# Performance work log

Measured on AMD Instinct MI355X. Metric: run time of the kernel, lower is better.

Reference implementation:

```python
import jax, jax.numpy as jnp
import numpy as np

N, E, IN, OUT, R, B = 20000, 640000, 256, 800, 8, 8


def setup_inputs() -> dict:
    key = jax.random.key(0)
    k0, k1, k2, k3, k4, k5 = jax.random.split(key, 6)
    x = jax.random.normal(k0, (N, IN), dtype=jnp.float32)
    edge_index = jax.random.randint(k1, (2, E), 0, N, dtype=jnp.int32)
    edge_type = jax.random.randint(k2, (E,), 0, R, dtype=jnp.int32)
    # basis-decomposed relation weights: W_r = sum_b att[r,b] * bases[b]
    bases = jax.random.normal(k3, (B, IN, OUT), dtype=jnp.float32) * 0.05
    att = jax.random.normal(k4, (R, B), dtype=jnp.float32) * 0.3
    root = jax.random.normal(k5, (IN, OUT), dtype=jnp.float32) * 0.05
    bias = jnp.zeros((OUT,), dtype=jnp.float32)
    return {"x": x, "edge_index": edge_index, "edge_type": edge_type,
            "bases": bases, "att": att, "root": root, "bias": bias}


def reference(x, edge_index, edge_type, bases, att, root, bias):
    # RGCNConv (basis decomposition, scatter-add aggregation):
    #   out[v] = sum_{(u->v, r) in edges} x[u] @ W_r  +  x[v] @ root  +  bias
    # Efficient form: first segment-sum x[src] per (dst, relation), then one
    # dense contraction with the R relation weights (math-identical for add-aggr).
    n, in_dim = x.shape
    r, b = att.shape
    W = jnp.einsum('rb,bio->rio', att, bases)          # [R, IN, OUT]
    src, dst = edge_index[0], edge_index[1]
    seg = dst.astype(jnp.int32) * r + edge_type.astype(jnp.int32)
    # per-(node, relation) sums of source features: [N*R, IN] -> [N, R, IN]
    s = jax.ops.segment_sum(x[src], seg, num_segments=n * r).reshape(n, r, in_dim)
    out = jnp.einsum('nri,rio->no', s, W) + x @ root + bias
    return out
```

## Files before the change

### kernel.cpp

```cpp
#include <hip/hip_runtime.h>


#define N_NODES 20000
#define N_EDGES 640000
#define IN_DIM  256
#define OUT_DIM 800
#define NREL    8
#define NSEG    160000
#define KS      2048
#define KTOT    2304
#define NPAD    1024
#define NB      625

#define BM 128
#define BN 256
#define BK 64
#define NKT (KTOT / BK)
#define MT  157
#define NT  4
#define NWG (MT * NT)
#define LBUF 49152

typedef float f32x4_t __attribute__((ext_vector_type(4)));
typedef short short8_t __attribute__((ext_vector_type(8)));

__device__ __forceinline__ unsigned short f2bf(float f) {
  unsigned u = __float_as_uint(f);
  u += 0x7fffu + ((u >> 16) & 1u);
  return (unsigned short)(u >> 16);
}

__device__ __forceinline__ float bflo(unsigned w) { return __uint_as_float(w << 16); }
__device__ __forceinline__ float bfhi(unsigned w) { return __uint_as_float(w & 0xffff0000u); }

__device__ __forceinline__ void gload16(const void* g, void* l) {
  __builtin_amdgcn_global_load_lds(
      (const __attribute__((address_space(1))) void*)g,
      (__attribute__((address_space(3))) void*)l, 16, 0, 0);
}


__global__ void zero_counts_kernel(int* __restrict__ cnt) {
  cnt[blockIdx.x * 256 + threadIdx.x] = 0;
}

__global__ void hist_kernel(const int* __restrict__ ei, const int* __restrict__ et,
                            int* __restrict__ cnt) {
  const int e = blockIdx.x * 256 + threadIdx.x;
  const int seg = ei[N_EDGES + e] * NREL + et[e];
  atomicAdd(&cnt[seg], 1);
}

__global__ void scan_reduce_kernel(const int* __restrict__ cnt, int* __restrict__ bsum) {
  __shared__ int sm[256];
  const int t = threadIdx.x;
  sm[t] = cnt[blockIdx.x * 256 + t];
  __syncthreads();
  for (int s = 128; s > 0; s >>= 1) {
    if (t < s) sm[t] += sm[t + s];
    __syncthreads();
  }
  if (t == 0) bsum[blockIdx.x] = sm[0];
}

__global__ void scan_bsum_kernel(int* __restrict__ bsum) {
  __shared__ int sm[1024];
  const int t = threadIdx.x;
  const int v = (t < NB) ? bsum[t] : 0;
  sm[t] = v;
  __syncthreads();
  for (int s = 1; s < 1024; s <<= 1) {
    const int a = (t >= s) ? sm[t - s] : 0;
    __syncthreads();
    sm[t] += a;
    __syncthreads();
  }
  if (t < NB) bsum[t] = sm[t] - v;
}

__global__ void scan_final_kernel(const int* __restrict__ cnt, const int* __restrict__ bsum,
                                  int* __restrict__ off, int* __restrict__ cur) {
  __shared__ int sm[256];
  const int t = threadIdx.x;
  const int g = blockIdx.x * 256 + t;
  const int v = cnt[g];
  sm[t] = v;
  __syncthreads();
  for (int s = 1; s < 256; s <<= 1) {
    const int a = (t >= s) ? sm[t - s] : 0;
    __syncthreads();
    sm[t] += a;
    __syncthreads();
  }
  const int ex = sm[t] - v + bsum[blockIdx.x];
  off[g] = ex;
  cur[g] = ex;
}

__global__ void reorder_kernel(const int* __restrict__ ei, const int* __restrict__ et,
                               int* __restrict__ cur, int* __restrict__ sorted_src) {
  const int e = blockIdx.x * 256 + threadIdx.x;
  const int seg = ei[N_EDGES + e] * NREL + et[e];
  const int pos = atomicAdd(&cur[seg], 1);
  sorted_src[pos] = ei[e];
}

__global__ void xcast_kernel(const float* __restrict__ x, unsigned short* __restrict__ abf) {
  const int id = blockIdx.x * 256 + threadIdx.x;
  const int row = id >> 6, lane = id & 63;
  const float4 v = ((const float4*)x)[(size_t)row * 64 + lane];
  union { unsigned short u[4]; uint2 q; } pk;
  pk.u[0] = f2bf(v.x); pk.u[1] = f2bf(v.y);
  pk.u[2] = f2bf(v.z); pk.u[3] = f2bf(v.w);
  *(uint2*)(abf + (size_t)row * KTOT + KS + lane * 4) = pk.q;
}

__global__ void aggregate_kernel(const int* __restrict__ cnt, const int* __restrict__ off,
                                 const int* __restrict__ sorted_src,
                                 unsigned short* __restrict__ abf) {
  const int wv = blockIdx.x * 4 + (threadIdx.x >> 6);
  const int l = threadIdx.x & 63;
  const int seg = wv * 2 + (l >> 5);
  const int sl = l & 31;
  const int ne = cnt[seg];
  const int o  = off[seg];
  float a0 = 0.f, a1 = 0.f, a2 = 0.f, a3 = 0.f;
  float a4 = 0.f, a5 = 0.f, a6 = 0.f, a7 = 0.f;
  float c0 = 0.f, c1 = 0.f, c2 = 0.f, c3 = 0.f;
  float c4 = 0.f, c5 = 0.f, c6 = 0.f, c7 = 0.f;
  int j = 0;
  for (; j + 1 < ne; j += 2) {
    const int s0 = sorted_src[o + j];
    const int s1 = sorted_src[o + j + 1];
    const uint4 u = *(const uint4*)(abf + (size_t)s0 * KTOT + KS + sl * 8);
    const uint4 v = *(const uint4*)(abf + (size_t)s1 * KTOT + KS + sl * 8);
    a0 += bflo(u.x); a1 += bfhi(u.x); a2 += bflo(u.y); a3 += bfhi(u.y);
    a4 += bflo(u.z); a5 += bfhi(u.z); a6 += bflo(u.w); a7 += bfhi(u.w);
    c0 += bflo(v.x); c1 += bfhi(v.x); c2 += bflo(v.y); c3 += bfhi(v.y);
    c4 += bflo(v.z); c5 += bfhi(v.z); c6 += bflo(v.w); c7 += bfhi(v.w);
  }
  if (j < ne) {
    const uint4 u = *(const uint4*)(abf + (size_t)sorted_src[o + j] * KTOT + KS + sl * 8);
    a0 += bflo(u.x); a1 += bfhi(u.x); a2 += bflo(u.y); a3 += bfhi(u.y);
    a4 += bflo(u.z); a5 += bfhi(u.z); a6 += bflo(u.w); a7 += bfhi(u.w);
  }
  a0 += c0; a1 += c1; a2 += c2; a3 += c3;
  a4 += c4; a5 += c5; a6 += c6; a7 += c7;
  const int node = seg >> 3, r = seg & 7;
  union { unsigned short u[8]; uint4 q; } pk;
  pk.u[0] = f2bf(a0); pk.u[1] = f2bf(a1); pk.u[2] = f2bf(a2); pk.u[3] = f2bf(a3);
  pk.u[4] = f2bf(a4); pk.u[5] = f2bf(a5); pk.u[6] = f2bf(a6); pk.u[7] = f2bf(a7);
  *(uint4*)(abf + (size_t)node * KTOT + r * IN_DIM + sl * 8) = pk.q;
}

__global__ void build_wcat_kernel(const float* __restrict__ bases,
                                  const float* __restrict__ att,
                                  const float* __restrict__ root,
                                  unsigned short* __restrict__ wcatT) {
  const int k = blockIdx.x;
  const int n = blockIdx.y * 128 + threadIdx.x;
  float v = 0.f;
  if (n < OUT_DIM) {
    if (k < KS) {
      const int r = k >> 8, i = k & 255;
      #pragma unroll
      for (int b = 0; b < 8; ++b)
        v += att[r * 8 + b] * bases[((size_t)b * IN_DIM + i) * OUT_DIM + n];
    } else {
      v = root[(size_t)(k - KS) * OUT_DIM + n];
    }
  }
  wcatT[(size_t)n * KTOT + k] = f2bf(v);
}

__global__ __launch_bounds__(512) void gemm_kernel(
    const unsigned short* __restrict__ abf,
    const unsigned short* __restrict__ wcatT,
    const float* __restrict__ bias, float* __restrict__ out) {
  __shared__ __align__(16) char lds[3 * LBUF];

  const int lin = blockIdx.x;
  const int q8 = NWG >> 3, r8 = NWG & 7;
  const int xcd = lin & 7, idx = lin >> 3;
  const int wg = (xcd < r8 ? xcd * (q8 + 1) : r8 * (q8 + 1) + (xcd - r8) * q8) + idx;
  const int row0 = (wg % MT) * BM;
  const int col0 = (wg / MT) * BN;

  const int tid = threadIdx.x;
  const int w = tid >> 6, l = tid & 63;
  const int wm = w >> 2, wn = w & 3;
  const int la = l & 15, lg = l >> 4;
  const int l3 = l >> 3;
  const int sch = (l & 7) ^ l3;

  const unsigned short* gA[2];
  const unsigned short* gB[4];
  #pragma unroll
  for (int i = 0; i < 2; ++i) {
    int ga = row0 + i * 64 + w * 8 + l3;
    ga = (ga < N_NODES) ? ga : (N_NODES - 1);
    gA[i] = abf + (size_t)ga * KTOT + sch * 8;
  }
  #pragma unroll
  for (int i = 0; i < 4; ++i)
    gB[i] = wcatT + (size_t)(col0 + i * 64 + w * 8 + l3) * KTOT + sch * 8;

  f32x4_t acc[4][4];
  #pragma unroll
  for (int i = 0; i < 4; ++i)
    #pragma unroll
    for (int j = 0; j < 4; ++j)
      acc[i][j] = (f32x4_t)(0.0f);

  auto stage_all = [&](int buf, int kt) {
    char* pA = lds + buf * LBUF + w * 1024;
    char* pB = pA + 16384;
    const int ko = kt * BK;
    gload16(gA[0] + ko, pA);
    gload16(gA[1] + ko, pA + 8192);
    gload16(gB[0] + ko, pB);
    gload16(gB[1] + ko, pB + 8192);
    gload16(gB[2] + ko, pB + 16384);
    gload16(gB[3] + ko, pB + 24576);
  };

  stage_all(0, 0);
  stage_all(1, 1);

  for (int kt = 0; kt < NKT; ++kt) {
    const int cbuf = kt % 3;
    const int pbuf = (kt + 2) % 3;
    const bool pf = (kt + 2) < NKT;
    const int pko = (kt + 2) * BK;
    const char* Ab = lds + cbuf * LBUF;
    const char* Bb = Ab + 16384;
    char* pA = lds + pbuf * LBUF + w * 1024;
    char* pB = pA + 16384;

    if (kt + 1 < NKT) { asm volatile("s_waitcnt vmcnt(6)" ::: "memory"); }
    else              { asm volatile("s_waitcnt vmcnt(0)" ::: "memory"); }
    __builtin_amdgcn_sched_barrier(0);
    __builtin_amdgcn_s_barrier();

    short8_t af0, af1, bf0, bf1, bf2, bf3;

    {
      const int r0 = wm * 64 + la,       r1 = wm * 64 + 16 + la;
      af0 = *(const short8_t*)(Ab + r0 * 128 + ((lg << 4) ^ ((r0 & 7) << 4)));
      af1 = *(const short8_t*)(Ab + r1 * 128 + ((lg << 4) ^ ((r1 & 7) << 4)));
      #pragma unroll
      for (int nf = 0; nf < 4; ++nf) {
        const int rr = wn * 64 + nf * 16 + la;
        const short8_t v = *(const short8_t*)(Bb + rr * 128 + ((lg << 4) ^ ((rr & 7) << 4)));
        if (nf == 0) bf0 = v; else if (nf == 1) bf1 = v; else if (nf == 2) bf2 = v; else bf3 = v;
      }
      if (pf) { gload16(gA[0] + pko, pA); gload16(gA[1] + pko, pA + 8192); }
      __builtin_amdgcn_s_barrier();
      asm volatile("s_waitcnt lgkmcnt(0)" ::: "memory");
      __builtin_amdgcn_sched_barrier(0);
      __builtin_amdgcn_s_setprio(1);
      acc[0][0] = __builtin_amdgcn_mfma_f32_16x16x32_bf16(af0, bf0, acc[0][0], 0, 0, 0);
      acc[0][1] = __builtin_amdgcn_mfma_f32_16x16x32_bf16(af0, bf1, acc[0][1], 0, 0, 0);
      acc[0][2] = __builtin_amdgcn_mfma_f32_16x16x32_bf16(af0, bf2, acc[0][2], 0, 0, 0);
      acc[0][3] = __builtin_amdgcn_mfma_f32_16x16x32_bf16(af0, bf3, acc[0][3], 0, 0, 0);
      acc[1][0] = __builtin_amdgcn_mfma_f32_16x16x32_bf16(af1, bf0, acc[1][0], 0, 0, 0);
      acc[1][1] = __builtin_amdgcn_mfma_f32_16x16x32_bf16(af1, bf1, acc[1][1], 0, 0, 0);
      acc[1][2] = __builtin_amdgcn_mfma_f32_16x16x32_bf16(af1, bf2, acc[1][2], 0, 0, 0);
      acc[1][3] = __builtin_amdgcn_mfma_f32_16x16x32_bf16(af1, bf3, acc[1][3], 0, 0, 0);
      __builtin_amdgcn_s_setprio(0);
      __builtin_amdgcn_s_barrier();
    }
    {
      const int r0 = wm * 64 + 32 + la,  r1 = wm * 64 + 48 + la;
      af0 = *(const short8_t*)(Ab + r0 * 128 + ((lg << 4) ^ ((r0 & 7) << 4)));
      af1 = *(const short8_t*)(Ab + r1 * 128 + ((lg << 4) ^ ((r1 & 7) << 4)));
      if (pf) { gload16(gB[0] + pko, pB); gload16(gB[1] + pko, pB + 8192); }
      __builtin_amdgcn_s_barrier();
      asm volatile("s_waitcnt lgkmcnt(0)" ::: "memory");
      __builtin_amdgcn_sched_barrier(0);
      __builtin_amdgcn_s_setprio(1);
      acc[2][0] = __builtin_amdgcn_mfma_f32_16x16x32_bf16(af0, bf0, acc[2][0], 0, 0, 0);
      acc[2][1] = __builtin_amdgcn_mfma_f32_16x16x32_bf16(af0, bf1, acc[2][1], 0, 0, 0);
      acc[2][2] = __builtin_amdgcn_mfma_f32_16x16x32_bf16(af0, bf2, acc[2][2], 0, 0, 0);
      acc[2][3] = __builtin_amdgcn_mfma_f32_16x16x32_bf16(af0, bf3, acc[2][3], 0, 0, 0);
      acc[3][0] = __builtin_amdgcn_mfma_f32_16x16x32_bf16(af1, bf0, acc[3][0], 0, 0, 0);
      acc[3][1] = __builtin_amdgcn_mfma_f32_16x16x32_bf16(af1, bf1, acc[3][1], 0, 0, 0);
      acc[3][2] = __builtin_amdgcn_mfma_f32_16x16x32_bf16(af1, bf2, acc[3][2], 0, 0, 0);
      acc[3][3] = __builtin_amdgcn_mfma_f32_16x16x32_bf16(af1, bf3, acc[3][3], 0, 0, 0);
      __builtin_amdgcn_s_setprio(0);
      __builtin_amdgcn_s_barrier();
    }
    {
      const int r0 = wm * 64 + la,       r1 = wm * 64 + 16 + la;
      af0 = *(const short8_t*)(Ab + r0 * 128 + (((4 + lg) << 4) ^ ((r0 & 7) << 4)));
      af1 = *(const short8_t*)(Ab + r1 * 128 + (((4 + lg) << 4) ^ ((r1 & 7) << 4)));
      #pragma unroll
      for (int nf = 0; nf < 4; ++nf) {
        const int rr = wn * 64 + nf * 16 + la;
        const short8_t v = *(const short8_t*)(Bb + rr * 128 + (((4 + lg) << 4) ^ ((rr & 7) << 4)));
        if (nf == 0) bf0 = v; else if (nf == 1) bf1 = v; else if (nf == 2) bf2 = v; else bf3 = v;
      }
      if (pf) { gload16(gB[2] + pko, pB + 16384); gload16(gB[3] + pko, pB + 24576); }
      __builtin_amdgcn_s_barrier();
      asm volatile("s_waitcnt lgkmcnt(0)" ::: "memory");
      __builtin_amdgcn_sched_barrier(0);
      __builtin_amdgcn_s_setprio(1);
      acc[0][0] = __builtin_amdgcn_mfma_f32_16x16x32_bf16(af0, bf0, acc[0][0], 0, 0, 0);
      acc[0][1] = __builtin_amdgcn_mfma_f32_16x16x32_bf16(af0, bf1, acc[0][1], 0, 0, 0);
      acc[0][2] = __builtin_amdgcn_mfma_f32_16x16x32_bf16(af0, bf2, acc[0][2], 0, 0, 0);
      acc[0][3] = __builtin_amdgcn_mfma_f32_16x16x32_bf16(af0, bf3, acc[0][3], 0, 0, 0);
      acc[1][0] = __builtin_amdgcn_mfma_f32_16x16x32_bf16(af1, bf0, acc[1][0], 0, 0, 0);
      acc[1][1] = __builtin_amdgcn_mfma_f32_16x16x32_bf16(af1, bf1, acc[1][1], 0, 0, 0);
      acc[1][2] = __builtin_amdgcn_mfma_f32_16x16x32_bf16(af1, bf2, acc[1][2], 0, 0, 0);
      acc[1][3] = __builtin_amdgcn_mfma_f32_16x16x32_bf16(af1, bf3, acc[1][3], 0, 0, 0);
      __builtin_amdgcn_s_setprio(0);
      __builtin_amdgcn_s_barrier();
    }
    {
      const int r0 = wm * 64 + 32 + la,  r1 = wm * 64 + 48 + la;
      af0 = *(const short8_t*)(Ab + r0 * 128 + (((4 + lg) << 4) ^ ((r0 & 7) << 4)));
      af1 = *(const short8_t*)(Ab + r1 * 128 + (((4 + lg) << 4) ^ ((r1 & 7) << 4)));
      __builtin_amdgcn_s_barrier();
      asm volatile("s_waitcnt lgkmcnt(0)" ::: "memory");
      __builtin_amdgcn_sched_barrier(0);
      __builtin_amdgcn_s_setprio(1);
      acc[2][0] = __builtin_amdgcn_mfma_f32_16x16x32_bf16(af0, bf0, acc[2][0], 0, 0, 0);
      acc[2][1] = __builtin_amdgcn_mfma_f32_16x16x32_bf16(af0, bf1, acc[2][1], 0, 0, 0);
      acc[2][2] = __builtin_amdgcn_mfma_f32_16x16x32_bf16(af0, bf2, acc[2][2], 0, 0, 0);
      acc[2][3] = __builtin_amdgcn_mfma_f32_16x16x32_bf16(af0, bf3, acc[2][3], 0, 0, 0);
      acc[3][0] = __builtin_amdgcn_mfma_f32_16x16x32_bf16(af1, bf0, acc[3][0], 0, 0, 0);
      acc[3][1] = __builtin_amdgcn_mfma_f32_16x16x32_bf16(af1, bf1, acc[3][1], 0, 0, 0);
      acc[3][2] = __builtin_amdgcn_mfma_f32_16x16x32_bf16(af1, bf2, acc[3][2], 0, 0, 0);
      acc[3][3] = __builtin_amdgcn_mfma_f32_16x16x32_bf16(af1, bf3, acc[3][3], 0, 0, 0);
      __builtin_amdgcn_s_setprio(0);
      __builtin_amdgcn_s_barrier();
    }
  }

  #pragma unroll
  for (int nf = 0; nf < 4; ++nf) {
    const int gcol = col0 + wn * 64 + nf * 16 + la;
    if (gcol < OUT_DIM) {
      const float bv = bias[gcol];
      #pragma unroll
      for (int f = 0; f < 4; ++f) {
        const int gr0 = row0 + wm * 64 + f * 16 + lg * 4;
        #pragma unroll
        for (int j = 0; j < 4; ++j) {
          const int gr = gr0 + j;
          if (gr < N_NODES)
            out[(size_t)gr * OUT_DIM + gcol] = acc[f][nf][j] + bv;
        }
      }
    }
  }
}

extern "C" void kernel_launch(void* const* d_in, const int* in_sizes, int n_in,
                              void* d_out, int out_size, void* d_ws, size_t ws_size,
                              hipStream_t stream) {
  const float* x     = (const float*)d_in[0];
  const int*   ei    = (const int*)d_in[1];
  const int*   et    = (const int*)d_in[2];
  const float* bases = (const float*)d_in[3];
  const float* att   = (const float*)d_in[4];
  const float* root  = (const float*)d_in[5];
  const float* bias  = (const float*)d_in[6];
  float* out = (float*)d_out;

  char* p = (char*)d_ws;
  unsigned short* abf   = (unsigned short*)p;  p += (size_t)N_NODES * KTOT * 2;
  unsigned short* wcatT = (unsigned short*)p;  p += (size_t)NPAD * KTOT * 2;
  int* cnt        = (int*)p;                   p += (size_t)NSEG * 4;
  int* off        = (int*)p;                   p += (size_t)NSEG * 4;
  int* cur        = (int*)p;                   p += (size_t)NSEG * 4;
  int* sorted_src = (int*)p;                   p += (size_t)N_EDGES * 4;
  int* bsum       = (int*)p;                   p += 4096;

  zero_counts_kernel<<<NB, 256, 0, stream>>>(cnt);
  hist_kernel<<<N_EDGES / 256, 256, 0, stream>>>(ei, et, cnt);
  scan_reduce_kernel<<<NB, 256, 0, stream>>>(cnt, bsum);
  scan_bsum_kernel<<<1, 1024, 0, stream>>>(bsum);
  scan_final_kernel<<<NB, 256, 0, stream>>>(cnt, bsum, off, cur);
  reorder_kernel<<<N_EDGES / 256, 256, 0, stream>>>(ei, et, cur, sorted_src);
  xcast_kernel<<<N_NODES * 64 / 256, 256, 0, stream>>>(x, abf);
  aggregate_kernel<<<NSEG / 8, 256, 0, stream>>>(cnt, off, sorted_src, abf);
  build_wcat_kernel<<<dim3(KTOT, 8), 128, 0, stream>>>(bases, att, root, wcatT);
  gemm_kernel<<<NWG, 512, 0, stream>>>(abf, wcatT, bias, out);
}
```

Before: 269.4 us.

## Halve GEMM K-tile, switch to k-major LDS layout, skip dead-column waves

Halves the GEMM K step from 64 to 32 and shrinks each LDS buffer to match. The A/B staging becomes a k-group-major layout with one global-to-LDS load per operand slice, replacing the XOR-swizzled row layout. The four barrier-separated sub-phases per iteration collapse into one prefetch plus two MFMA groups. Waves whose output columns fall past OUT_DIM skip their LDS reads and MFMAs, which removes wasted work in the padded last column tile. In exchange there are twice as many K iterations, each with its own barrier and wait. The new unswizzled layout, with lanes reading 16-byte rows at 16-byte stride, may cause LDS bank conflicts.

```diff
diff --git a/kernel.cpp b/kernel.cpp
--- a/kernel.cpp
+++ b/kernel.cpp
@@ -14,12 +14,12 @@
 
 #define BM 128
 #define BN 256
-#define BK 64
+#define BK 32
 #define NKT (KTOT / BK)
 #define MT  157
 #define NT  4
 #define NWG (MT * NT)
-#define LBUF 49152
+#define LBUF 24576
 
 typedef float f32x4_t __attribute__((ext_vector_type(4)));
 typedef short short8_t __attribute__((ext_vector_type(8)));
@@ -190,20 +190,12 @@
   const int w = tid >> 6, l = tid & 63;
   const int wm = w >> 2, wn = w & 3;
   const int la = l & 15, lg = l >> 4;
-  const int l3 = l >> 3;
-  const int sch = (l & 7) ^ l3;
-
-  const unsigned short* gA[2];
-  const unsigned short* gB[4];
-  #pragma unroll
-  for (int i = 0; i < 2; ++i) {
-    int ga = row0 + i * 64 + w * 8 + l3;
-    ga = (ga < N_NODES) ? ga : (N_NODES - 1);
-    gA[i] = abf + (size_t)ga * KTOT + sch * 8;
-  }
-  #pragma unroll
-  for (int i = 0; i < 4; ++i)
-    gB[i] = wcatT + (size_t)(col0 + i * 64 + w * 8 + l3) * KTOT + sch * 8;
+
+  int raw = row0 + (tid & 127);
+  raw = (raw < N_NODES) ? raw : (N_NODES - 1);
+  const unsigned short* gA  = abf   + (size_t)raw * KTOT + (tid >> 7) * 8;
+  const unsigned short* gB0 = wcatT + (size_t)(col0 + (tid & 255)) * KTOT + (tid >> 8) * 8;
+  const unsigned short* gB1 = gB0 + 16;
 
   f32x4_t acc[4][4];
   #pragma unroll
@@ -212,50 +204,42 @@
     for (int j = 0; j < 4; ++j)
       acc[i][j] = (f32x4_t)(0.0f);
 
-  auto stage_all = [&](int buf, int kt) {
-    char* pA = lds + buf * LBUF + w * 1024;
-    char* pB = pA + 16384;
+  const bool wactive = (col0 + wn * 64) < OUT_DIM;
+
+  auto stage = [&](int buf, int kt) {
+    char* base = lds + buf * LBUF;
     const int ko = kt * BK;
-    gload16(gA[0] + ko, pA);
-    gload16(gA[1] + ko, pA + 8192);
-    gload16(gB[0] + ko, pB);
-    gload16(gB[1] + ko, pB + 8192);
-    gload16(gB[2] + ko, pB + 16384);
-    gload16(gB[3] + ko, pB + 24576);
+    gload16(gA  + ko, base + w * 1024);
+    gload16(gB0 + ko, base + 8192 + w * 1024);
+    gload16(gB1 + ko, base + 8192 + 8192 + w * 1024);
   };
 
-  stage_all(0, 0);
-  stage_all(1, 1);
-
+  stage(0, 0);
+  stage(1, 1);
+
+  int cbuf = 0;
   for (int kt = 0; kt < NKT; ++kt) {
-    const int cbuf = kt % 3;
-    const int pbuf = (kt + 2) % 3;
-    const bool pf = (kt + 2) < NKT;
-    const int pko = (kt + 2) * BK;
-    const char* Ab = lds + cbuf * LBUF;
-    const char* Bb = Ab + 16384;
-    char* pA = lds + pbuf * LBUF + w * 1024;
-    char* pB = pA + 16384;
-
-    if (kt + 1 < NKT) { asm volatile("s_waitcnt vmcnt(6)" ::: "memory"); }
+    if (kt + 1 < NKT) { asm volatile("s_waitcnt vmcnt(3)" ::: "memory"); }
     else              { asm volatile("s_waitcnt vmcnt(0)" ::: "memory"); }
     __builtin_amdgcn_sched_barrier(0);
     __builtin_amdgcn_s_barrier();
-
-    short8_t af0, af1, bf0, bf1, bf2, bf3;
-
-    {
-      const int r0 = wm * 64 + la,       r1 = wm * 64 + 16 + la;
-      af0 = *(const short8_t*)(Ab + r0 * 128 + ((lg << 4) ^ ((r0 & 7) << 4)));
-      af1 = *(const short8_t*)(Ab + r1 * 128 + ((lg << 4) ^ ((r1 & 7) << 4)));
-      #pragma unroll
-      for (int nf = 0; nf < 4; ++nf) {
-        const int rr = wn * 64 + nf * 16 + la;
-        const short8_t v = *(const short8_t*)(Bb + rr * 128 + ((lg << 4) ^ ((rr & 7) << 4)));
-        if (nf == 0) bf0 = v; else if (nf == 1) bf1 = v; else if (nf == 2) bf2 = v; else bf3 = v;
-      }
-      if (pf) { gload16(gA[0] + pko, pA); gload16(gA[1] + pko, pA + 8192); }
-      __builtin_amdgcn_s_barrier();
+    __builtin_amdgcn_sched_barrier(0);
+
+    if (kt + 2 < NKT) {
+      const int pbuf = (cbuf + 2 >= 3) ? cbuf - 1 : cbuf + 2;
+      stage(pbuf, kt + 2);
+    }
+
+    if (wactive) {
+      const char* Ab = lds + cbuf * LBUF;
+      const char* Bb = Ab + 8192;
+      short8_t af0, af1, bf0, bf1, bf2, bf3;
+      af0 = *(const short8_t*)(Ab + lg * 2048 + (wm * 64      + la) * 16);
+      af1 = *(const short8_t*)(Ab + lg * 2048 + (wm * 64 + 16 + la) * 16);
+      bf0 = *(const short8_t*)(Bb + lg * 4096 + (wn * 64      + la) * 16);
+      bf1 = *(const short8_t*)(Bb + lg * 4096 + (wn * 64 + 16 + la) * 16);
+      bf2 = *(const short8_t*)(Bb + lg * 4096 + (wn * 64 + 32 + la) * 16);
+      bf3 = *(const short8_t*)(Bb + lg * 4096 + (wn * 64 + 48 + la) * 16);
       asm volatile("s_waitcnt lgkmcnt(0)" ::: "memory");
       __builtin_amdgcn_sched_barrier(0);
       __builtin_amdgcn_s_setprio(1);
@@ -268,14 +252,8 @@
       acc[1][2] = __builtin_amdgcn_mfma_f32_16x16x32_bf16(af1, bf2, acc[1][2], 0, 0, 0);
       acc[1][3] = __builtin_amdgcn_mfma_f32_16x16x32_bf16(af1, bf3, acc[1][3], 0, 0, 0);
       __builtin_amdgcn_s_setprio(0);
-      __builtin_amdgcn_s_barrier();
-    }
-    {
-      const int r0 = wm * 64 + 32 + la,  r1 = wm * 64 + 48 + la;
-      af0 = *(const short8_t*)(Ab + r0 * 128 + ((lg << 4) ^ ((r0 & 7) << 4)));
-      af1 = *(const short8_t*)(Ab + r1 * 128 + ((lg << 4) ^ ((r1 & 7) << 4)));
-      if (pf) { gload16(gB[0] + pko, pB); gload16(gB[1] + pko, pB + 8192); }
-      __builtin_amdgcn_s_barrier();
+      af0 = *(const short8_t*)(Ab + lg * 2048 + (wm * 64 + 32 + la) * 16);
+      af1 = *(const short8_t*)(Ab + lg * 2048 + (wm * 64 + 48 + la) * 16);
       asm volatile("s_waitcnt lgkmcnt(0)" ::: "memory");
       __builtin_amdgcn_sched_barrier(0);
       __builtin_amdgcn_s_setprio(1);
@@ -288,68 +266,25 @@
       acc[3][2] = __builtin_amdgcn_mfma_f32_16x16x32_bf16(af1, bf2, acc[3][2], 0, 0, 0);
       acc[3][3] = __builtin_amdgcn_mfma_f32_16x16x32_bf16(af1, bf3, acc[3][3], 0, 0, 0);
       __builtin_amdgcn_s_setprio(0);
-      __builtin_amdgcn_s_barrier();
     }
-    {
-      const int r0 = wm * 64 + la,       r1 = wm * 64 + 16 + la;
-      af0 = *(const short8_t*)(Ab + r0 * 128 + (((4 + lg) << 4) ^ ((r0 & 7) << 4)));
-      af1 = *(const short8_t*)(Ab + r1 * 128 + (((4 + lg) << 4) ^ ((r1 & 7) << 4)));
-      #pragma unroll
-      for (int nf = 0; nf < 4; ++nf) {
-        const int rr = wn * 64 + nf * 16 + la;
-        const short8_t v = *(const short8_t*)(Bb + rr * 128 + (((4 + lg) << 4) ^ ((rr & 7) << 4)));
-        if (nf == 0) bf0 = v; else if (nf == 1) bf1 = v; else if (nf == 2) bf2 = v; else bf3 = v;
-      }
-      if (pf) { gload16(gB[2] + pko, pB + 16384); gload16(gB[3] + pko, pB + 24576); }
-      __builtin_amdgcn_s_barrier();
-      asm volatile("s_waitcnt lgkmcnt(0)" ::: "memory");
-      __builtin_amdgcn_sched_barrier(0);
-      __builtin_amdgcn_s_setprio(1);
-      acc[0][0] = __builtin_amdgcn_mfma_f32_16x16x32_bf16(af0, bf0, acc[0][0], 0, 0, 0);
-      acc[0][1] = __builtin_amdgcn_mfma_f32_16x16x32_bf16(af0, bf1, acc[0][1], 0, 0, 0);
-      acc[0][2] = __builtin_amdgcn_mfma_f32_16x16x32_bf16(af0, bf2, acc[0][2], 0, 0, 0);
-      acc[0][3] = __builtin_amdgcn_mfma_f32_16x16x32_bf16(af0, bf3, acc[0][3], 0, 0, 0);
-      acc[1][0] = __builtin_amdgcn_mfma_f32_16x16x32_bf16(af1, bf0, acc[1][0], 0, 0, 0);
-      acc[1][1] = __builtin_amdgcn_mfma_f32_16x16x32_bf16(af1, bf1, acc[1][1], 0, 0, 0);
-      acc[1][2] = __builtin_amdgcn_mfma_f32_16x16x32_bf16(af1, bf2, acc[1][2], 0, 0, 0);
-      acc[1][3] = __builtin_amdgcn_mfma_f32_16x16x32_bf16(af1, bf3, acc[1][3], 0, 0, 0);
-      __builtin_amdgcn_s_setprio(0);
-      __builtin_amdgcn_s_barrier();
-    }
-    {
-      const int r0 = wm * 64 + 32 + la,  r1 = wm * 64 + 48 + la;
-      af0 = *(const short8_t*)(Ab + r0 * 128 + (((4 + lg) << 4) ^ ((r0 & 7) << 4)));
-      af1 = *(const short8_t*)(Ab + r1 * 128 + (((4 + lg) << 4) ^ ((r1 & 7) << 4)));
-      __builtin_amdgcn_s_barrier();
-      asm volatile("s_waitcnt lgkmcnt(0)" ::: "memory");
-      __builtin_amdgcn_sched_barrier(0);
-      __builtin_amdgcn_s_setprio(1);
-      acc[2][0] = __builtin_amdgcn_mfma_f32_16x16x32_bf16(af0, bf0, acc[2][0], 0, 0, 0);
-      acc[2][1] = __builtin_amdgcn_mfma_f32_16x16x32_bf16(af0, bf1, acc[2][1], 0, 0, 0);
-      acc[2][2] = __builtin_amdgcn_mfma_f32_16x16x32_bf16(af0, bf2, acc[2][2], 0, 0, 0);
-      acc[2][3] = __builtin_amdgcn_mfma_f32_16x16x32_bf16(af0, bf3, acc[2][3], 0, 0, 0);
-      acc[3][0] = __builtin_amdgcn_mfma_f32_16x16x32_bf16(af1, bf0, acc[3][0], 0, 0, 0);
-      acc[3][1] = __builtin_amdgcn_mfma_f32_16x16x32_bf16(af1, bf1, acc[3][1], 0, 0, 0);
-      acc[3][2] = __builtin_amdgcn_mfma_f32_16x16x32_bf16(af1, bf2, acc[3][2], 0, 0, 0);
-      acc[3][3] = __builtin_amdgcn_mfma_f32_16x16x32_bf16(af1, bf3, acc[3][3], 0, 0, 0);
-      __builtin_amdgcn_s_setprio(0);
-      __builtin_amdgcn_s_barrier();
-    }
-  }
-
-  #pragma unroll
-  for (int nf = 0; nf < 4; ++nf) {
-    const int gcol = col0 + wn * 64 + nf * 16 + la;
-    if (gcol < OUT_DIM) {
-      const float bv = bias[gcol];
-      #pragma unroll
-      for (int f = 0; f < 4; ++f) {
-        const int gr0 = row0 + wm * 64 + f * 16 + lg * 4;
+    cbuf = (cbuf + 1 >= 3) ? 0 : cbuf + 1;
+  }
+
+  if (wactive) {
+    #pragma unroll
+    for (int nf = 0; nf < 4; ++nf) {
+      const int gcol = col0 + wn * 64 + nf * 16 + la;
+      if (gcol < OUT_DIM) {
+        const float bv = bias[gcol];
         #pragma unroll
-        for (int j = 0; j < 4; ++j) {
-          const int gr = gr0 + j;
-          if (gr < N_NODES)
-            out[(size_t)gr * OUT_DIM + gcol] = acc[f][nf][j] + bv;
+        for (int f = 0; f < 4; ++f) {
+          const int gr0 = row0 + wm * 64 + f * 16 + lg * 4;
+          #pragma unroll
+          for (int j = 0; j < 4; ++j) {
+            const int gr = gr0 + j;
+            if (gr < N_NODES)
+              out[(size_t)gr * OUT_DIM + gcol] = acc[f][nf][j] + bv;
+          }
         }
       }
     }
```

After: 381.1 us. 1.41x slower.
